# Kernel optimization log

Hardware: AMD Instinct MI355X
Metric: run time of the kernel (lower is better)

Reference implementation:

```python
import jax, jax.numpy as jnp
import numpy as np

N = 50000
E = 800000
H = 128


def _lin_init(key, fan_in, fan_out):
    s = 1.0 / np.sqrt(fan_in)
    k1, k2 = jax.random.split(key)
    W = jax.random.uniform(k1, (fan_in, fan_out), minval=-s, maxval=s, dtype=jnp.float32)
    b = jax.random.uniform(k2, (fan_out,), minval=-s, maxval=s, dtype=jnp.float32)
    return W, b


def setup_inputs() -> dict:
    key = jax.random.key(0)
    ks = jax.random.split(key, 24)
    inp = {}
    inp['x'] = jax.random.normal(ks[0], (N, 1), dtype=jnp.float32)
    inp['edge_attr'] = jax.random.normal(ks[1], (E, 1), dtype=jnp.float32)
    inp['q_Y_sample'] = jax.random.normal(ks[2], (E, 1), dtype=jnp.float32)
    inp['adj'] = jax.random.randint(ks[3], (2, E), 0, N, dtype=jnp.int32)
    inp['t'] = jax.random.uniform(ks[4], (1,), dtype=jnp.float32) * 1000.0
    inp['num_steps'] = 1000
    inp['batch'] = jnp.zeros((N,), dtype=jnp.int32)
    # parameters
    inp['We'], inp['be'] = _lin_init(ks[5], 1, H // 2)      # edge_map
    inp['Wo'], inp['bo'] = _lin_init(ks[6], 1, H // 2)      # edge_map_opt
    inp['Wl1'], inp['bl1'] = _lin_init(ks[7], H, 1)         # conv1 edge lin (edge_dim->in_channels)
    inp['Wn1'], inp['bn1'] = _lin_init(ks[8], 1, H)         # conv1 nn
    inp['Wl2'], inp['bl2'] = _lin_init(ks[9], H, H)         # conv2 edge lin
    inp['Wn2'], inp['bn2'] = _lin_init(ks[10], H, H)        # conv2 nn
    inp['Wl3'], inp['bl3'] = _lin_init(ks[11], H, H)        # conv3 edge lin
    inp['Wn3'], inp['bn3'] = _lin_init(ks[12], H, H)        # conv3 nn
    inp['Wt1'], inp['bt1'] = _lin_init(ks[13], H, 2 * H)    # time_mlp[0]
    inp['Wt2'], inp['bt2'] = _lin_init(ks[14], 2 * H, H)    # time_mlp[2]
    inp['Wd1'], inp['bd1'] = _lin_init(ks[15], 257, 257)    # decode[0]
    inp['Wd2'], inp['bd2'] = _lin_init(ks[16], 257, 1)      # decode[2]
    return inp


def reference(x, edge_attr, q_Y_sample, adj, t, num_steps, batch,
              We, be, Wo, bo,
              Wl1, bl1, Wn1, bn1, Wl2, bl2, Wn2, bn2, Wl3, bl3, Wn3, bn3,
              Wt1, bt1, Wt2, bt2, Wd1, bd1, Wd2, bd2):
    n = x.shape[0]
    src, dst = adj[0], adj[1]
    # edge embedding: cat(edge_map(edge_attr), edge_map_opt(q_Y_sample)) -> [E, 128]
    ee = jnp.concatenate([edge_attr @ We + be, q_Y_sample @ Wo + bo], axis=-1)
    # sinusoidal time embedding (t/num_steps*num_steps*rescale == 4*t)
    half = H // 2
    freqs = jnp.exp(jnp.arange(half, dtype=jnp.float32) * (-np.log(10000.0) / (half - 1)))
    tv = (t * 4.0)[:, None] * freqs[None, :]
    temb = jnp.concatenate([jnp.sin(tv), jnp.cos(tv)], axis=-1)  # [1, 128]
    temb = jax.nn.relu(temb @ Wt1 + bt1) @ Wt2 + bt2              # [1, 128], broadcasts to [N, 128]

    def gine(h, Wl, bl, Wn, bn):
        # PyG GINEConv (eps=0): out = nn(x + sum_j relu(x_j + lin(edge_attr)))
        m = jax.nn.relu(h[src] + (ee @ Wl + bl))                  # [E, d_in]
        agg = jax.ops.segment_sum(m, dst, num_segments=n)         # [N, d_in]
        return (h + agg) @ Wn + bn

    h = gine(x, Wl1, bl1, Wn1, bn1) + temb
    h = gine(h, Wl2, bl2, Wn2, bn2) + temb
    h = gine(h, Wl3, bl3, Wn3, bn3) + temb
    # decode on edges: cat(h[src], h[dst], q_Y_sample) -> MLP -> [E, 1]
    z = jnp.concatenate([h[src], h[dst], q_Y_sample], axis=-1)    # [E, 257]
    return jax.nn.relu(z @ Wd1 + bd1) @ Wd2 + bd2
```

## Files before the change

### kernel.cpp

```cpp
#include <hip/hip_runtime.h>

typedef unsigned int uint;
typedef unsigned short ushort;

#define AB_U 132

typedef __attribute__((ext_vector_type(8))) short short8;
typedef __attribute__((ext_vector_type(4))) float f32x4;
union U4S8 { uint4 u; short8 s; };

__device__ __forceinline__ ushort f2bf(float f) {
    uint u = __float_as_uint(f);
    u += 0x7FFFu + ((u >> 16) & 1u);
    return (ushort)(u >> 16);
}
__device__ __forceinline__ float bf2f_lo(uint p) { return __uint_as_float(p << 16); }
__device__ __forceinline__ float bf2f_hi(uint p) { return __uint_as_float(p & 0xFFFF0000u); }
__device__ __forceinline__ uint packbf(float lo, float hi) {
    return (uint)f2bf(lo) | ((uint)f2bf(hi) << 16);
}

__global__ __launch_bounds__(256) void precompute_kernel(
    const float* __restrict__ t,
    const float* __restrict__ We, const float* __restrict__ be,
    const float* __restrict__ Wo, const float* __restrict__ bo,
    const float* __restrict__ Wl1, const float* __restrict__ bl1,
    const float* __restrict__ Wl2, const float* __restrict__ bl2,
    const float* __restrict__ Wl3, const float* __restrict__ bl3,
    const float* __restrict__ Wt1, const float* __restrict__ bt1,
    const float* __restrict__ Wt2, const float* __restrict__ bt2,
    float* __restrict__ wsmall)
{
    __shared__ float t0[128];
    __shared__ float y1[256];
    int tid = threadIdx.x;
    float tt = t[0] * 4.0f;
    if (tid < 64) {
        float f = expf(-logf(10000.0f) * (float)tid / 63.0f);
        float v = tt * f;
        t0[tid]      = sinf(v);
        t0[tid + 64] = cosf(v);
    }
    __syncthreads();
    {
        float acc = bt1[tid];
        for (int k = 0; k < 128; k++) acc = fmaf(t0[k], Wt1[k * 256 + tid], acc);
        y1[tid] = fmaxf(acc, 0.0f);
    }
    __syncthreads();
    if (tid < 128) {
        float a = bt2[tid];
        for (int k = 0; k < 256; k++) a = fmaf(y1[k], Wt2[k * 128 + tid], a);
        wsmall[tid] = a;
    }
    {
        int j = tid & 127;
        const float* Wl  = (tid < 128) ? Wl2 : Wl3;
        const float* blp = (tid < 128) ? bl2 : bl3;
        float p = 0.f, q = 0.f, r = blp[j];
        for (int k = 0; k < 64; k++) {
            float w1 = Wl[k * 128 + j], w2 = Wl[(64 + k) * 128 + j];
            p = fmaf(We[k], w1, p);
            q = fmaf(Wo[k], w2, q);
            r = fmaf(be[k], w1, r);
            r = fmaf(bo[k], w2, r);
        }
        int base = (tid < 128) ? 128 : 512;
        wsmall[base + j]       = p;
        wsmall[base + 128 + j] = q;
        wsmall[base + 256 + j] = r;
    }
    if (tid == 0) {
        float p1 = 0.f, q1 = 0.f, r1 = bl1[0];
        for (int k = 0; k < 64; k++) {
            p1 = fmaf(We[k], Wl1[k], p1);
            q1 = fmaf(Wo[k], Wl1[64 + k], q1);
            r1 = fmaf(be[k], Wl1[k], r1);
            r1 = fmaf(bo[k], Wl1[64 + k], r1);
        }
        wsmall[896] = p1; wsmall[897] = q1; wsmall[898] = r1;
    }
}

__global__ __launch_bounds__(64) void wt16_kernel(
    const float* __restrict__ Wd1, uint* __restrict__ Wt16u)
{
    int c = blockIdx.x;
    int u = threadIdx.x;
    int k = u * 2;
    float lo, hi;
    if (c < 256) {
        lo = Wd1[k * 257 + c];
        hi = Wd1[(k + 1) * 257 + c];
    } else {
        int cc = c - 256;
        lo = Wd1[(128 + k) * 257 + cc];
        hi = Wd1[(128 + k + 1) * 257 + cc];
    }
    Wt16u[c * 64 + u] = packbf(lo, hi);
}

__global__ __launch_bounds__(256) void hist_kernel(
    const int* __restrict__ dst, int* __restrict__ cnt, int E)
{
    int e = blockIdx.x * blockDim.x + threadIdx.x;
    if (e < E) atomicAdd(&cnt[dst[e]], 1);
}

__global__ __launch_bounds__(256) void scan1_kernel(
    const int* __restrict__ cnt, int* __restrict__ rowstart,
    int* __restrict__ partials, int N)
{
    __shared__ int wsum[4];
    int b = blockIdx.x;
    int tid = threadIdx.x, lane = tid & 63, w = tid >> 6;
    int i0 = b * 1024 + tid * 4;
    int v0 = (i0     < N) ? cnt[i0]     : 0;
    int v1 = (i0 + 1 < N) ? cnt[i0 + 1] : 0;
    int v2 = (i0 + 2 < N) ? cnt[i0 + 2] : 0;
    int v3 = (i0 + 3 < N) ? cnt[i0 + 3] : 0;
    int tsum = v0 + v1 + v2 + v3;
    int s = tsum;
#pragma unroll
    for (int off = 1; off < 64; off <<= 1) {
        int u = __shfl_up(s, off, 64);
        if (lane >= off) s += u;
    }
    if (lane == 63) wsum[w] = s;
    __syncthreads();
    int woff = 0;
    for (int k = 0; k < w; k++) woff += wsum[k];
    int ex = woff + s - tsum;
    if (i0     < N) rowstart[i0]     = ex;
    if (i0 + 1 < N) rowstart[i0 + 1] = ex + v0;
    if (i0 + 2 < N) rowstart[i0 + 2] = ex + v0 + v1;
    if (i0 + 3 < N) rowstart[i0 + 3] = ex + v0 + v1 + v2;
    if (tid == 255) partials[b] = woff + s;
}

__global__ __launch_bounds__(64) void scan2_kernel(
    int* __restrict__ partials, int* __restrict__ rowstart, int nblk, int N)
{
    int lane = threadIdx.x;
    int carry = 0;
    for (int base = 0; base < nblk; base += 64) {
        int i = base + lane;
        int v = (i < nblk) ? partials[i] : 0;
        int s = v;
#pragma unroll
        for (int off = 1; off < 64; off <<= 1) {
            int u = __shfl_up(s, off, 64);
            if (lane >= off) s += u;
        }
        if (i < nblk) partials[i] = carry + s - v;
        carry += __shfl(s, 63, 64);
    }
    if (lane == 0) rowstart[N] = carry;
}

__global__ __launch_bounds__(256) void scan3_kernel(
    int* __restrict__ rowstart, const int* __restrict__ partials, int N)
{
    int i = blockIdx.x * blockDim.x + threadIdx.x;
    if (i < N) rowstart[i] += partials[i >> 10];
}

__global__ __launch_bounds__(256) void scatter_kernel(
    const int* __restrict__ src, const int* __restrict__ dst,
    const float* __restrict__ ea, const float* __restrict__ qy,
    const int* __restrict__ rowstart, int* __restrict__ cursor,
    uint4* __restrict__ epack, int E)
{
    int e = blockIdx.x * blockDim.x + threadIdx.x;
    if (e >= E) return;
    int d = dst[e];
    int pos = atomicAdd(&cursor[d], 1);
    uint4 pk;
    pk.x = (uint)e;
    pk.y = (uint)src[e];
    pk.z = __float_as_uint(ea[e]);
    pk.w = __float_as_uint(qy[e]);
    epack[rowstart[d] + pos] = pk;
}

__global__ __launch_bounds__(256) void edge1_kernel(
    const float* __restrict__ x, const uint4* __restrict__ epack,
    const int* __restrict__ rowstart, const float* __restrict__ scal,
    float* __restrict__ agg1, int N)
{
    int v = blockIdx.x * blockDim.x + threadIdx.x;
    if (v >= N) return;
    float s0 = scal[0], s1 = scal[1], s2 = scal[2];
    int beg = rowstart[v], end = rowstart[v + 1];
    float m = 0.0f;
    int i = beg;
    for (; i + 2 <= end; i += 2) {
        uint4 pk0 = epack[i];
        uint4 pk1 = epack[i + 1];
        float x0 = x[(int)pk0.y];
        float x1 = x[(int)pk1.y];
        m += fmaxf(x0 + fmaf(__uint_as_float(pk0.z), s0, fmaf(__uint_as_float(pk0.w), s1, s2)), 0.0f);
        m += fmaxf(x1 + fmaf(__uint_as_float(pk1.z), s0, fmaf(__uint_as_float(pk1.w), s1, s2)), 0.0f);
    }
    if (i < end) {
        uint4 pk = epack[i];
        m += fmaxf(x[(int)pk.y] + fmaf(__uint_as_float(pk.z), s0, fmaf(__uint_as_float(pk.w), s1, s2)), 0.0f);
    }
    agg1[v] = m;
}

__global__ __launch_bounds__(256) void node1_kernel(
    const float* __restrict__ x, const float* __restrict__ agg1,
    const float* __restrict__ Wn1, const float* __restrict__ bn1,
    const float* __restrict__ temb, float* __restrict__ h,
    uint* __restrict__ h16u, int N)
{
    int i = blockIdx.x * blockDim.x + threadIdx.x;
    int n = i >> 6, j2 = (i & 63) * 2;
    if (n >= N) return;
    float v = x[n] + agg1[n];
    float h0 = fmaf(v, Wn1[j2],     bn1[j2]     + temb[j2]);
    float h1 = fmaf(v, Wn1[j2 + 1], bn1[j2 + 1] + temb[j2 + 1]);
    *(float2*)(h + (size_t)n * 128 + j2) = make_float2(h0, h1);
    h16u[(size_t)n * 64 + (j2 >> 1)] = packbf(h0, h1);
}

__global__ __launch_bounds__(256) void aggL_kernel(
    const uint* __restrict__ h16u, const uint4* __restrict__ epack,
    const int* __restrict__ rowstart,
    const float* __restrict__ P, const float* __restrict__ Q,
    const float* __restrict__ R, float* __restrict__ agg, int N)
{
    int v = blockIdx.x * 4 + (threadIdx.x >> 6);
    int lane = threadIdx.x & 63;
    if (v >= N) return;
    int c = lane * 2;
    float2 Pv = *(const float2*)(P + c);
    float2 Qv = *(const float2*)(Q + c);
    float2 Rv = *(const float2*)(R + c);
    int beg = rowstart[v], end = rowstart[v + 1];
    float accx = 0.0f, accy = 0.0f;
    int i = beg;
    for (; i + 4 <= end; i += 4) {
        uint4 pk0 = epack[i];
        uint4 pk1 = epack[i + 1];
        uint4 pk2 = epack[i + 2];
        uint4 pk3 = epack[i + 3];
        uint hp0 = h16u[(size_t)pk0.y * 64 + lane];
        uint hp1 = h16u[(size_t)pk1.y * 64 + lane];
        uint hp2 = h16u[(size_t)pk2.y * 64 + lane];
        uint hp3 = h16u[(size_t)pk3.y * 64 + lane];
        float a0 = __uint_as_float(pk0.z), b0 = __uint_as_float(pk0.w);
        float a1 = __uint_as_float(pk1.z), b1 = __uint_as_float(pk1.w);
        float a2 = __uint_as_float(pk2.z), b2 = __uint_as_float(pk2.w);
        float a3 = __uint_as_float(pk3.z), b3 = __uint_as_float(pk3.w);
        accx += fmaxf(bf2f_lo(hp0) + fmaf(a0, Pv.x, fmaf(b0, Qv.x, Rv.x)), 0.0f);
        accy += fmaxf(bf2f_hi(hp0) + fmaf(a0, Pv.y, fmaf(b0, Qv.y, Rv.y)), 0.0f);
        accx += fmaxf(bf2f_lo(hp1) + fmaf(a1, Pv.x, fmaf(b1, Qv.x, Rv.x)), 0.0f);
        accy += fmaxf(bf2f_hi(hp1) + fmaf(a1, Pv.y, fmaf(b1, Qv.y, Rv.y)), 0.0f);
        accx += fmaxf(bf2f_lo(hp2) + fmaf(a2, Pv.x, fmaf(b2, Qv.x, Rv.x)), 0.0f);
        accy += fmaxf(bf2f_hi(hp2) + fmaf(a2, Pv.y, fmaf(b2, Qv.y, Rv.y)), 0.0f);
        accx += fmaxf(bf2f_lo(hp3) + fmaf(a3, Pv.x, fmaf(b3, Qv.x, Rv.x)), 0.0f);
        accy += fmaxf(bf2f_hi(hp3) + fmaf(a3, Pv.y, fmaf(b3, Qv.y, Rv.y)), 0.0f);
    }
    for (; i < end; i++) {
        uint4 pk = epack[i];
        float a = __uint_as_float(pk.z), b = __uint_as_float(pk.w);
        uint hp = h16u[(size_t)pk.y * 64 + lane];
        accx += fmaxf(bf2f_lo(hp) + fmaf(a, Pv.x, fmaf(b, Qv.x, Rv.x)), 0.0f);
        accy += fmaxf(bf2f_hi(hp) + fmaf(a, Pv.y, fmaf(b, Qv.y, Rv.y)), 0.0f);
    }
    *(float2*)(agg + (size_t)v * 128 + c) = make_float2(accx, accy);
}

__global__ __launch_bounds__(256) void nodeL_kernel(
    float* __restrict__ h, const float* __restrict__ agg,
    const float* __restrict__ W, const float* __restrict__ bn,
    const float* __restrict__ temb, uint* __restrict__ h16u, int N)
{
    __shared__ float vs[64][128];
    int nb = blockIdx.x * 64;
    int tid = threadIdx.x;
    for (int idx = tid; idx < 64 * 32; idx += 256) {
        int n = idx >> 5, c = (idx & 31) * 4;
        float4 a = make_float4(0.f, 0.f, 0.f, 0.f);
        if (nb + n < N) {
            a = *(const float4*)(h + (size_t)(nb + n) * 128 + c);
            float4 g = *(const float4*)(agg + (size_t)(nb + n) * 128 + c);
            a.x += g.x; a.y += g.y; a.z += g.z; a.w += g.w;
        }
        *(float4*)(&vs[n][c]) = a;
    }
    __syncthreads();
    int o0 = (tid & 31) * 4;
    int n0 = (tid >> 5) * 8;
    float acc[8][4];
    float4 bb = *(const float4*)(bn + o0);
    float4 tb = *(const float4*)(temb + o0);
    bb.x += tb.x; bb.y += tb.y; bb.z += tb.z; bb.w += tb.w;
#pragma unroll
    for (int i = 0; i < 8; i++) {
        acc[i][0] = bb.x; acc[i][1] = bb.y; acc[i][2] = bb.z; acc[i][3] = bb.w;
    }
    for (int k = 0; k < 128; k += 4) {
        float hv[8][4];
#pragma unroll
        for (int i = 0; i < 8; i++)
            *(float4*)hv[i] = *(const float4*)(&vs[n0 + i][k]);
#pragma unroll
        for (int kk = 0; kk < 4; kk++) {
            float4 wv = *(const float4*)(W + (k + kk) * 128 + o0);
#pragma unroll
            for (int i = 0; i < 8; i++) {
                float hvv = hv[i][kk];
                acc[i][0] = fmaf(hvv, wv.x, acc[i][0]);
                acc[i][1] = fmaf(hvv, wv.y, acc[i][1]);
                acc[i][2] = fmaf(hvv, wv.z, acc[i][2]);
                acc[i][3] = fmaf(hvv, wv.w, acc[i][3]);
            }
        }
    }
#pragma unroll
    for (int i = 0; i < 8; i++) {
        int n = nb + n0 + i;
        if (n < N) {
            *(float4*)(h + (size_t)n * 128 + o0) =
                make_float4(acc[i][0], acc[i][1], acc[i][2], acc[i][3]);
            uint2 pk;
            pk.x = packbf(acc[i][0], acc[i][1]);
            pk.y = packbf(acc[i][2], acc[i][3]);
            *(uint2*)(h16u + (size_t)n * 64 + (o0 >> 1)) = pk;
        }
    }
}

__global__ __launch_bounds__(256) void node3_decode_kernel(
    const float* __restrict__ h, const float* __restrict__ agg,
    const float* __restrict__ Wn3, const float* __restrict__ bn3,
    const float* __restrict__ temb, const uint* __restrict__ Wt16u,
    const float* __restrict__ Wd1, const float* __restrict__ bd1,
    ushort* __restrict__ A16s, ushort* __restrict__ B16s, int N)
{
    __shared__ float vs[16][128];
    __shared__ uint hs16[16][68];
    int nb = blockIdx.x * 16;
    int tid = threadIdx.x;
    for (int idx = tid; idx < 16 * 32; idx += 256) {
        int n = idx >> 5, c = (idx & 31) * 4;
        float4 a = make_float4(0.f, 0.f, 0.f, 0.f);
        if (nb + n < N) {
            a = *(const float4*)(h + (size_t)(nb + n) * 128 + c);
            float4 g = *(const float4*)(agg + (size_t)(nb + n) * 128 + c);
            a.x += g.x; a.y += g.y; a.z += g.z; a.w += g.w;
        }
        *(float4*)(&vs[n][c]) = a;
    }
    __syncthreads();
    {
        int o0 = (tid & 31) * 4;
        int n0 = (tid >> 5) * 2;
        float acc[2][4];
        float4 bb = *(const float4*)(bn3 + o0);
        float4 tb = *(const float4*)(temb + o0);
        bb.x += tb.x; bb.y += tb.y; bb.z += tb.z; bb.w += tb.w;
#pragma unroll
        for (int i = 0; i < 2; i++) {
            acc[i][0] = bb.x; acc[i][1] = bb.y; acc[i][2] = bb.z; acc[i][3] = bb.w;
        }
        for (int k = 0; k < 128; k += 4) {
            float hv0[4], hv1[4];
            *(float4*)hv0 = *(const float4*)(&vs[n0][k]);
            *(float4*)hv1 = *(const float4*)(&vs[n0 + 1][k]);
#pragma unroll
            for (int kk = 0; kk < 4; kk++) {
                float4 wv = *(const float4*)(Wn3 + (k + kk) * 128 + o0);
                acc[0][0] = fmaf(hv0[kk], wv.x, acc[0][0]);
                acc[0][1] = fmaf(hv0[kk], wv.y, acc[0][1]);
                acc[0][2] = fmaf(hv0[kk], wv.z, acc[0][2]);
                acc[0][3] = fmaf(hv0[kk], wv.w, acc[0][3]);
                acc[1][0] = fmaf(hv1[kk], wv.x, acc[1][0]);
                acc[1][1] = fmaf(hv1[kk], wv.y, acc[1][1]);
                acc[1][2] = fmaf(hv1[kk], wv.z, acc[1][2]);
                acc[1][3] = fmaf(hv1[kk], wv.w, acc[1][3]);
            }
        }
#pragma unroll
        for (int i = 0; i < 2; i++) {
            uint2 pk;
            pk.x = packbf(acc[i][0], acc[i][1]);
            pk.y = packbf(acc[i][2], acc[i][3]);
            *(uint2*)(&hs16[n0 + i][o0 >> 1]) = pk;
        }
    }
    __syncthreads();
    {
        int wv = tid >> 6;
        int lane = tid & 63;
        int cl = lane & 15;
        int g = lane >> 4;
        short8 afr[4];
#pragma unroll
        for (int kc = 0; kc < 4; kc++) {
            U4S8 t;
            t.u = *(const uint4*)(&hs16[cl][kc * 16 + g * 4]);
            afr[kc] = t.s;
        }
#pragma unroll
        for (int tt = 0; tt < 8; tt++) {
            int tile = wv * 8 + tt;
            int c = tile * 16 + cl;
            float bias = (tile < 16) ? bd1[c] : 0.0f;
            f32x4 acc = {bias, bias, bias, bias};
#pragma unroll
            for (int kc = 0; kc < 4; kc++) {
                U4S8 t;
                t.u = *(const uint4*)(Wt16u + (size_t)c * 64 + kc * 16 + g * 4);
                acc = __builtin_amdgcn_mfma_f32_16x16x32_bf16(afr[kc], t.s, acc, 0, 0, 0);
            }
            ushort* OUT = (tile < 16) ? A16s : B16s;
            int oc = (tile < 16) ? c : (c - 256);
#pragma unroll
            for (int r = 0; r < 4; r++) {
                int n = nb + g * 4 + r;
                if (n < N) OUT[(size_t)n * 264 + oc] = f2bf(acc[r]);
            }
        }
    }
    if (tid < 16) {
        int n = tid;
        float sA = bd1[256], sB = 0.f;
        for (int u = 0; u < 64; u++) {
            uint pk = hs16[n][u];
            float h0 = bf2f_lo(pk), h1 = bf2f_hi(pk);
            int k = u * 2;
            sA = fmaf(h0, Wd1[k * 257 + 256], sA);
            sA = fmaf(h1, Wd1[(k + 1) * 257 + 256], sA);
            sB = fmaf(h0, Wd1[(128 + k) * 257 + 256], sB);
            sB = fmaf(h1, Wd1[(128 + k + 1) * 257 + 256], sB);
        }
        if (nb + n < N) {
            A16s[(size_t)(nb + n) * 264 + 256] = f2bf(sA);
            B16s[(size_t)(nb + n) * 264 + 256] = f2bf(sB);
        }
    }
}

__global__ __launch_bounds__(256) void decodeE_kernel(
    const uint* __restrict__ A16u, const uint* __restrict__ B16u,
    const uint4* __restrict__ epack, const int* __restrict__ rowstart,
    const float* __restrict__ Wd1, const float* __restrict__ Wd2,
    const float* __restrict__ bd2, float* __restrict__ out, int N)
{
    int v = blockIdx.x * 4 + (threadIdx.x >> 6);
    int lane = threadIdx.x & 63;
    if (v >= N) return;
    const float* w256 = Wd1 + 256 * 257;
    float4 w2v = *(const float4*)(w256 + lane * 4);
    float4 wdv = *(const float4*)(Wd2 + lane * 4);
    const uint* Br = B16u + (size_t)v * AB_U;
    uint2 bp = *(const uint2*)(Br + lane * 2);
    float Bv0 = bf2f_lo(bp.x), Bv1 = bf2f_hi(bp.x);
    float Bv2 = bf2f_lo(bp.y), Bv3 = bf2f_hi(bp.y);
    float w2_l = w256[256], wd_l = Wd2[256], bd = bd2[0];
    float B_l = bf2f_lo(Br[128]);
    int beg = rowstart[v], end = rowstart[v + 1];
    int i = beg;
    for (; i + 2 <= end; i += 2) {
        uint4 pk0 = epack[i];
        uint4 pk1 = epack[i + 1];
        float q0 = __uint_as_float(pk0.w);
        float q1 = __uint_as_float(pk1.w);
        const uint* Ar0 = A16u + (size_t)pk0.y * AB_U;
        const uint* Ar1 = A16u + (size_t)pk1.y * AB_U;
        uint2 ap0 = *(const uint2*)(Ar0 + lane * 2);
        uint2 ap1 = *(const uint2*)(Ar1 + lane * 2);
        float t0 = 0.f, t1 = 0.f;
        if (lane == 0) {
            t0 = bf2f_lo(Ar0[128]);
            t1 = bf2f_lo(Ar1[128]);
        }
        float y00 = bf2f_lo(ap0.x) + fmaf(q0, w2v.x, Bv0);
        float y01 = bf2f_hi(ap0.x) + fmaf(q0, w2v.y, Bv1);
        float y02 = bf2f_lo(ap0.y) + fmaf(q0, w2v.z, Bv2);
        float y03 = bf2f_hi(ap0.y) + fmaf(q0, w2v.w, Bv3);
        float acc0 = fmaxf(y00, 0.f) * wdv.x + fmaxf(y01, 0.f) * wdv.y
                   + fmaxf(y02, 0.f) * wdv.z + fmaxf(y03, 0.f) * wdv.w;
        float y10 = bf2f_lo(ap1.x) + fmaf(q1, w2v.x, Bv0);
        float y11 = bf2f_hi(ap1.x) + fmaf(q1, w2v.y, Bv1);
        float y12 = bf2f_lo(ap1.y) + fmaf(q1, w2v.z, Bv2);
        float y13 = bf2f_hi(ap1.y) + fmaf(q1, w2v.w, Bv3);
        float acc1 = fmaxf(y10, 0.f) * wdv.x + fmaxf(y11, 0.f) * wdv.y
                   + fmaxf(y12, 0.f) * wdv.z + fmaxf(y13, 0.f) * wdv.w;
        if (lane == 0) {
            acc0 = fmaf(fmaxf(t0 + fmaf(q0, w2_l, B_l), 0.f), wd_l, acc0);
            acc1 = fmaf(fmaxf(t1 + fmaf(q1, w2_l, B_l), 0.f), wd_l, acc1);
        }
#pragma unroll
        for (int off = 32; off > 0; off >>= 1) {
            acc0 += __shfl_xor(acc0, off, 64);
            acc1 += __shfl_xor(acc1, off, 64);
        }
        if (lane == 0) {
            out[(int)pk0.x] = acc0 + bd;
            out[(int)pk1.x] = acc1 + bd;
        }
    }
    if (i < end) {
        uint4 pk = epack[i];
        float q = __uint_as_float(pk.w);
        const uint* Ar = A16u + (size_t)pk.y * AB_U;
        uint2 ap = *(const uint2*)(Ar + lane * 2);
        float y0 = bf2f_lo(ap.x) + fmaf(q, w2v.x, Bv0);
        float y1 = bf2f_hi(ap.x) + fmaf(q, w2v.y, Bv1);
        float y2 = bf2f_lo(ap.y) + fmaf(q, w2v.z, Bv2);
        float y3 = bf2f_hi(ap.y) + fmaf(q, w2v.w, Bv3);
        float acc = fmaxf(y0, 0.f) * wdv.x + fmaxf(y1, 0.f) * wdv.y
                  + fmaxf(y2, 0.f) * wdv.z + fmaxf(y3, 0.f) * wdv.w;
        if (lane == 0) {
            float yl = bf2f_lo(Ar[128]) + fmaf(q, w2_l, B_l);
            acc = fmaf(fmaxf(yl, 0.f), wd_l, acc);
        }
#pragma unroll
        for (int off = 32; off > 0; off >>= 1) acc += __shfl_xor(acc, off, 64);
        if (lane == 0) out[(int)pk.x] = acc + bd;
    }
}

extern "C" void kernel_launch(void* const* d_in, const int* in_sizes, int n_in,
                              void* d_out, int out_size, void* d_ws, size_t ws_size,
                              hipStream_t stream) {
    (void)n_in; (void)out_size; (void)ws_size;
    const float* x   = (const float*)d_in[0];
    const float* ea  = (const float*)d_in[1];
    const float* qy  = (const float*)d_in[2];
    const int*   adj = (const int*)d_in[3];
    const float* t   = (const float*)d_in[4];
    const float* We  = (const float*)d_in[7];
    const float* be  = (const float*)d_in[8];
    const float* Wo  = (const float*)d_in[9];
    const float* bo  = (const float*)d_in[10];
    const float* Wl1 = (const float*)d_in[11];
    const float* bl1 = (const float*)d_in[12];
    const float* Wn1 = (const float*)d_in[13];
    const float* bn1 = (const float*)d_in[14];
    const float* Wl2 = (const float*)d_in[15];
    const float* bl2 = (const float*)d_in[16];
    const float* Wn2 = (const float*)d_in[17];
    const float* bn2 = (const float*)d_in[18];
    const float* Wl3 = (const float*)d_in[19];
    const float* bl3 = (const float*)d_in[20];
    const float* Wn3 = (const float*)d_in[21];
    const float* bn3 = (const float*)d_in[22];
    const float* Wt1 = (const float*)d_in[23];
    const float* bt1 = (const float*)d_in[24];
    const float* Wt2 = (const float*)d_in[25];
    const float* bt2 = (const float*)d_in[26];
    const float* Wd1 = (const float*)d_in[27];
    const float* bd1 = (const float*)d_in[28];
    const float* Wd2 = (const float*)d_in[29];
    const float* bd2 = (const float*)d_in[30];
    float* out = (float*)d_out;

    int N = in_sizes[0];
    int E = in_sizes[3] / 2;
    const int* src = adj;
    const int* dst = adj + E;

    float* w    = (float*)d_ws;
    float* temb = w;
    float* P2   = w + 128;
    float* Q2   = w + 256;
    float* R2   = w + 384;
    float* P3   = w + 512;
    float* Q3   = w + 640;
    float* R3   = w + 768;
    float* scal = w + 896;
    float* h    = w + 1024;
    float* agg  = h + (size_t)N * 128;
    uint*  h16u = (uint*)(agg + (size_t)N * 128);
    uint*  A16u = h16u + (size_t)N * 64;
    uint*  B16u = A16u + (size_t)N * AB_U;
    int* rowstart = (int*)(B16u + (size_t)N * AB_U);
    int* cursor   = rowstart + (N + 1);
    int* partials = cursor + N;
    int nblk = (N + 1023) / 1024;
    char* pcur = (char*)(partials + nblk + 1);
    pcur = (char*)(((uintptr_t)pcur + 15) & ~(uintptr_t)15);
    uint4* epack = (uint4*)pcur;
    uint* Wt16u = (uint*)(epack + E);

    hipMemsetAsync(cursor, 0, (size_t)N * sizeof(int), stream);
    hist_kernel<<<(E + 255) / 256, 256, 0, stream>>>(dst, cursor, E);
    scan1_kernel<<<nblk, 256, 0, stream>>>(cursor, rowstart, partials, N);
    scan2_kernel<<<1, 64, 0, stream>>>(partials, rowstart, nblk, N);
    scan3_kernel<<<(N + 255) / 256, 256, 0, stream>>>(rowstart, partials, N);
    hipMemsetAsync(cursor, 0, (size_t)N * sizeof(int), stream);
    scatter_kernel<<<(E + 255) / 256, 256, 0, stream>>>(src, dst, ea, qy, rowstart, cursor, epack, E);

    wt16_kernel<<<512, 64, 0, stream>>>(Wd1, Wt16u);
    precompute_kernel<<<1, 256, 0, stream>>>(t, We, be, Wo, bo, Wl1, bl1,
                                             Wl2, bl2, Wl3, bl3,
                                             Wt1, bt1, Wt2, bt2, w);
    edge1_kernel<<<(N + 255) / 256, 256, 0, stream>>>(x, epack, rowstart, scal, agg, N);
    node1_kernel<<<(N * 64 + 255) / 256, 256, 0, stream>>>(x, agg, Wn1, bn1, temb, h, h16u, N);
    aggL_kernel<<<(N + 3) / 4, 256, 0, stream>>>(h16u, epack, rowstart, P2, Q2, R2, agg, N);
    nodeL_kernel<<<(N + 63) / 64, 256, 0, stream>>>(h, agg, Wn2, bn2, temb, h16u, N);
    aggL_kernel<<<(N + 3) / 4, 256, 0, stream>>>(h16u, epack, rowstart, P3, Q3, R3, agg, N);
    node3_decode_kernel<<<(N + 15) / 16, 256, 0, stream>>>(h, agg, Wn3, bn3, temb, Wt16u,
                                                           Wd1, bd1,
                                                           (ushort*)A16u, (ushort*)B16u, N);
    decodeE_kernel<<<(N + 3) / 4, 256, 0, stream>>>(A16u, B16u, epack, rowstart, Wd1, Wd2, bd2, out, N);
}
```

Baseline: 573.5 us.

## Use bf16 MFMA for node GEMMs and keep hidden/aggregate state in bf16

Replaces the fp32 FMA loops in the layer-2 and layer-3 node linear layers with bf16 MFMA 16x16x32 instructions, using pre-transposed bf16 copies of Wn2 and Wn3 made by a new small kernel. The fp32 node-state buffer is removed and the aggregation output is stored as packed bf16, roughly halving that write and read traffic. The node-3 decode path now keeps the layer-3 result in fp32 shared memory and splits the extra-column dot product across 64 threads with shuffles. This trades accuracy, since hidden state and aggregates are rounded to bf16 at more points, for less memory traffic and compute in the node stages.

```diff
diff --git a/kernel.cpp b/kernel.cpp
--- a/kernel.cpp
+++ b/kernel.cpp
@@ -98,6 +98,13 @@
         hi = Wd1[(128 + k + 1) * 257 + cc];
     }
     Wt16u[c * 64 + u] = packbf(lo, hi);
+}
+
+__global__ __launch_bounds__(64) void wnt16_kernel(
+    const float* __restrict__ W, uint* __restrict__ Wt)
+{
+    int c = blockIdx.x, u = threadIdx.x;
+    Wt[c * 64 + u] = packbf(W[(2 * u) * 128 + c], W[(2 * u + 1) * 128 + c]);
 }
 
 __global__ __launch_bounds__(256) void hist_kernel(
@@ -212,8 +219,7 @@
 __global__ __launch_bounds__(256) void node1_kernel(
     const float* __restrict__ x, const float* __restrict__ agg1,
     const float* __restrict__ Wn1, const float* __restrict__ bn1,
-    const float* __restrict__ temb, float* __restrict__ h,
-    uint* __restrict__ h16u, int N)
+    const float* __restrict__ temb, uint* __restrict__ h16u, int N)
 {
     int i = blockIdx.x * blockDim.x + threadIdx.x;
     int n = i >> 6, j2 = (i & 63) * 2;
@@ -221,7 +227,6 @@
     float v = x[n] + agg1[n];
     float h0 = fmaf(v, Wn1[j2],     bn1[j2]     + temb[j2]);
     float h1 = fmaf(v, Wn1[j2 + 1], bn1[j2 + 1] + temb[j2 + 1]);
-    *(float2*)(h + (size_t)n * 128 + j2) = make_float2(h0, h1);
     h16u[(size_t)n * 64 + (j2 >> 1)] = packbf(h0, h1);
 }
 
@@ -229,7 +234,7 @@
     const uint* __restrict__ h16u, const uint4* __restrict__ epack,
     const int* __restrict__ rowstart,
     const float* __restrict__ P, const float* __restrict__ Q,
-    const float* __restrict__ R, float* __restrict__ agg, int N)
+    const float* __restrict__ R, uint* __restrict__ agg16u, int N)
 {
     int v = blockIdx.x * 4 + (threadIdx.x >> 6);
     int lane = threadIdx.x & 63;
@@ -270,139 +275,119 @@
         accx += fmaxf(bf2f_lo(hp) + fmaf(a, Pv.x, fmaf(b, Qv.x, Rv.x)), 0.0f);
         accy += fmaxf(bf2f_hi(hp) + fmaf(a, Pv.y, fmaf(b, Qv.y, Rv.y)), 0.0f);
     }
-    *(float2*)(agg + (size_t)v * 128 + c) = make_float2(accx, accy);
+    agg16u[(size_t)v * 64 + lane] = packbf(accx, accy);
 }
 
 __global__ __launch_bounds__(256) void nodeL_kernel(
-    float* __restrict__ h, const float* __restrict__ agg,
-    const float* __restrict__ W, const float* __restrict__ bn,
-    const float* __restrict__ temb, uint* __restrict__ h16u, int N)
-{
-    __shared__ float vs[64][128];
+    const uint* __restrict__ agg16u, const uint* __restrict__ Wn2t16u,
+    const float* __restrict__ bn, const float* __restrict__ temb,
+    uint* __restrict__ h16u, int N)
+{
+    __shared__ uint vs16[64][68];
     int nb = blockIdx.x * 64;
     int tid = threadIdx.x;
     for (int idx = tid; idx < 64 * 32; idx += 256) {
-        int n = idx >> 5, c = (idx & 31) * 4;
-        float4 a = make_float4(0.f, 0.f, 0.f, 0.f);
+        int n = idx >> 5, u2 = (idx & 31) * 2;
+        uint2 pk = make_uint2(0, 0);
         if (nb + n < N) {
-            a = *(const float4*)(h + (size_t)(nb + n) * 128 + c);
-            float4 g = *(const float4*)(agg + (size_t)(nb + n) * 128 + c);
-            a.x += g.x; a.y += g.y; a.z += g.z; a.w += g.w;
-        }
-        *(float4*)(&vs[n][c]) = a;
+            uint2 hp = *(const uint2*)(h16u + (size_t)(nb + n) * 64 + u2);
+            uint2 gp = *(const uint2*)(agg16u + (size_t)(nb + n) * 64 + u2);
+            pk.x = packbf(bf2f_lo(hp.x) + bf2f_lo(gp.x), bf2f_hi(hp.x) + bf2f_hi(gp.x));
+            pk.y = packbf(bf2f_lo(hp.y) + bf2f_lo(gp.y), bf2f_hi(hp.y) + bf2f_hi(gp.y));
+        }
+        *(uint2*)(&vs16[n][u2]) = pk;
     }
     __syncthreads();
-    int o0 = (tid & 31) * 4;
-    int n0 = (tid >> 5) * 8;
-    float acc[8][4];
-    float4 bb = *(const float4*)(bn + o0);
-    float4 tb = *(const float4*)(temb + o0);
-    bb.x += tb.x; bb.y += tb.y; bb.z += tb.z; bb.w += tb.w;
-#pragma unroll
-    for (int i = 0; i < 8; i++) {
-        acc[i][0] = bb.x; acc[i][1] = bb.y; acc[i][2] = bb.z; acc[i][3] = bb.w;
-    }
-    for (int k = 0; k < 128; k += 4) {
-        float hv[8][4];
-#pragma unroll
-        for (int i = 0; i < 8; i++)
-            *(float4*)hv[i] = *(const float4*)(&vs[n0 + i][k]);
-#pragma unroll
-        for (int kk = 0; kk < 4; kk++) {
-            float4 wv = *(const float4*)(W + (k + kk) * 128 + o0);
-#pragma unroll
-            for (int i = 0; i < 8; i++) {
-                float hvv = hv[i][kk];
-                acc[i][0] = fmaf(hvv, wv.x, acc[i][0]);
-                acc[i][1] = fmaf(hvv, wv.y, acc[i][1]);
-                acc[i][2] = fmaf(hvv, wv.z, acc[i][2]);
-                acc[i][3] = fmaf(hvv, wv.w, acc[i][3]);
-            }
-        }
-    }
-#pragma unroll
-    for (int i = 0; i < 8; i++) {
-        int n = nb + n0 + i;
-        if (n < N) {
-            *(float4*)(h + (size_t)n * 128 + o0) =
-                make_float4(acc[i][0], acc[i][1], acc[i][2], acc[i][3]);
-            uint2 pk;
-            pk.x = packbf(acc[i][0], acc[i][1]);
-            pk.y = packbf(acc[i][2], acc[i][3]);
-            *(uint2*)(h16u + (size_t)n * 64 + (o0 >> 1)) = pk;
+    int wv = tid >> 6, lane = tid & 63, cl = lane & 15, g = lane >> 4;
+    int rbase = wv * 16;
+    short8 afr[4];
+#pragma unroll
+    for (int kc = 0; kc < 4; kc++) {
+        U4S8 t;
+        t.u = *(const uint4*)(&vs16[rbase + cl][kc * 16 + g * 4]);
+        afr[kc] = t.s;
+    }
+#pragma unroll
+    for (int tt = 0; tt < 8; tt++) {
+        int c = tt * 16 + cl;
+        float bias = bn[c] + temb[c];
+        f32x4 acc = {bias, bias, bias, bias};
+#pragma unroll
+        for (int kc = 0; kc < 4; kc++) {
+            U4S8 t;
+            t.u = *(const uint4*)(Wn2t16u + (size_t)c * 64 + kc * 16 + g * 4);
+            acc = __builtin_amdgcn_mfma_f32_16x16x32_bf16(afr[kc], t.s, acc, 0, 0, 0);
+        }
+#pragma unroll
+        for (int r = 0; r < 4; r++) {
+            int n = nb + rbase + g * 4 + r;
+            float val = acc[r];
+            float nbr = __shfl_down(val, 1, 64);
+            if (n < N && (cl & 1) == 0)
+                h16u[(size_t)n * 64 + (c >> 1)] = packbf(val, nbr);
         }
     }
 }
 
 __global__ __launch_bounds__(256) void node3_decode_kernel(
-    const float* __restrict__ h, const float* __restrict__ agg,
-    const float* __restrict__ Wn3, const float* __restrict__ bn3,
+    const uint* __restrict__ h16u, const uint* __restrict__ agg16u,
+    const uint* __restrict__ Wn3t16u, const float* __restrict__ bn3,
     const float* __restrict__ temb, const uint* __restrict__ Wt16u,
     const float* __restrict__ Wd1, const float* __restrict__ bd1,
     ushort* __restrict__ A16s, ushort* __restrict__ B16s, int N)
 {
-    __shared__ float vs[16][128];
-    __shared__ uint hs16[16][68];
+    __shared__ uint vs16[16][68];
+    __shared__ float hs3[16][132];
     int nb = blockIdx.x * 16;
     int tid = threadIdx.x;
     for (int idx = tid; idx < 16 * 32; idx += 256) {
-        int n = idx >> 5, c = (idx & 31) * 4;
-        float4 a = make_float4(0.f, 0.f, 0.f, 0.f);
+        int n = idx >> 5, u2 = (idx & 31) * 2;
+        uint2 pk = make_uint2(0, 0);
         if (nb + n < N) {
-            a = *(const float4*)(h + (size_t)(nb + n) * 128 + c);
-            float4 g = *(const float4*)(agg + (size_t)(nb + n) * 128 + c);
-            a.x += g.x; a.y += g.y; a.z += g.z; a.w += g.w;
-        }
-        *(float4*)(&vs[n][c]) = a;
+            uint2 hp = *(const uint2*)(h16u + (size_t)(nb + n) * 64 + u2);
+            uint2 gp = *(const uint2*)(agg16u + (size_t)(nb + n) * 64 + u2);
+            pk.x = packbf(bf2f_lo(hp.x) + bf2f_lo(gp.x), bf2f_hi(hp.x) + bf2f_hi(gp.x));
+            pk.y = packbf(bf2f_lo(hp.y) + bf2f_lo(gp.y), bf2f_hi(hp.y) + bf2f_hi(gp.y));
+        }
+        *(uint2*)(&vs16[n][u2]) = pk;
+    }
+    __syncthreads();
+    int wv = tid >> 6, lane = tid & 63, cl = lane & 15, g = lane >> 4;
+    {
+        short8 afr[4];
+#pragma unroll
+        for (int kc = 0; kc < 4; kc++) {
+            U4S8 t;
+            t.u = *(const uint4*)(&vs16[cl][kc * 16 + g * 4]);
+            afr[kc] = t.s;
+        }
+#pragma unroll
+        for (int tt = 0; tt < 2; tt++) {
+            int c = wv * 32 + tt * 16 + cl;
+            float bias = bn3[c] + temb[c];
+            f32x4 acc = {bias, bias, bias, bias};
+#pragma unroll
+            for (int kc = 0; kc < 4; kc++) {
+                U4S8 t;
+                t.u = *(const uint4*)(Wn3t16u + (size_t)c * 64 + kc * 16 + g * 4);
+                acc = __builtin_amdgcn_mfma_f32_16x16x32_bf16(afr[kc], t.s, acc, 0, 0, 0);
+            }
+#pragma unroll
+            for (int r = 0; r < 4; r++) hs3[g * 4 + r][c] = acc[r];
+        }
     }
     __syncthreads();
     {
-        int o0 = (tid & 31) * 4;
-        int n0 = (tid >> 5) * 2;
-        float acc[2][4];
-        float4 bb = *(const float4*)(bn3 + o0);
-        float4 tb = *(const float4*)(temb + o0);
-        bb.x += tb.x; bb.y += tb.y; bb.z += tb.z; bb.w += tb.w;
-#pragma unroll
-        for (int i = 0; i < 2; i++) {
-            acc[i][0] = bb.x; acc[i][1] = bb.y; acc[i][2] = bb.z; acc[i][3] = bb.w;
-        }
-        for (int k = 0; k < 128; k += 4) {
-            float hv0[4], hv1[4];
-            *(float4*)hv0 = *(const float4*)(&vs[n0][k]);
-            *(float4*)hv1 = *(const float4*)(&vs[n0 + 1][k]);
-#pragma unroll
-            for (int kk = 0; kk < 4; kk++) {
-                float4 wv = *(const float4*)(Wn3 + (k + kk) * 128 + o0);
-                acc[0][0] = fmaf(hv0[kk], wv.x, acc[0][0]);
-                acc[0][1] = fmaf(hv0[kk], wv.y, acc[0][1]);
-                acc[0][2] = fmaf(hv0[kk], wv.z, acc[0][2]);
-                acc[0][3] = fmaf(hv0[kk], wv.w, acc[0][3]);
-                acc[1][0] = fmaf(hv1[kk], wv.x, acc[1][0]);
-                acc[1][1] = fmaf(hv1[kk], wv.y, acc[1][1]);
-                acc[1][2] = fmaf(hv1[kk], wv.z, acc[1][2]);
-                acc[1][3] = fmaf(hv1[kk], wv.w, acc[1][3]);
-            }
-        }
-#pragma unroll
-        for (int i = 0; i < 2; i++) {
-            uint2 pk;
-            pk.x = packbf(acc[i][0], acc[i][1]);
-            pk.y = packbf(acc[i][2], acc[i][3]);
-            *(uint2*)(&hs16[n0 + i][o0 >> 1]) = pk;
-        }
-    }
-    __syncthreads();
-    {
-        int wv = tid >> 6;
-        int lane = tid & 63;
-        int cl = lane & 15;
-        int g = lane >> 4;
         short8 afr[4];
 #pragma unroll
         for (int kc = 0; kc < 4; kc++) {
+            float4 lo = *(const float4*)(&hs3[cl][kc * 32 + g * 8]);
+            float4 hi = *(const float4*)(&hs3[cl][kc * 32 + g * 8 + 4]);
             U4S8 t;
-            t.u = *(const uint4*)(&hs16[cl][kc * 16 + g * 4]);
+            t.u.x = packbf(lo.x, lo.y);
+            t.u.y = packbf(lo.z, lo.w);
+            t.u.z = packbf(hi.x, hi.y);
+            t.u.w = packbf(hi.z, hi.w);
             afr[kc] = t.s;
         }
 #pragma unroll
@@ -426,20 +411,20 @@
             }
         }
     }
-    if (tid < 16) {
-        int n = tid;
-        float sA = bd1[256], sB = 0.f;
-        for (int u = 0; u < 64; u++) {
-            uint pk = hs16[n][u];
-            float h0 = bf2f_lo(pk), h1 = bf2f_hi(pk);
-            int k = u * 2;
-            sA = fmaf(h0, Wd1[k * 257 + 256], sA);
-            sA = fmaf(h1, Wd1[(k + 1) * 257 + 256], sA);
-            sB = fmaf(h0, Wd1[(128 + k) * 257 + 256], sB);
-            sB = fmaf(h1, Wd1[(128 + k + 1) * 257 + 256], sB);
-        }
-        if (nb + n < N) {
-            A16s[(size_t)(nb + n) * 264 + 256] = f2bf(sA);
+    if (tid < 64) {
+        int n = tid >> 2, j = tid & 3;
+        float sA = 0.f, sB = 0.f;
+        for (int k = j * 32; k < j * 32 + 32; k++) {
+            float hv = hs3[n][k];
+            sA = fmaf(hv, Wd1[k * 257 + 256], sA);
+            sB = fmaf(hv, Wd1[(128 + k) * 257 + 256], sB);
+        }
+        sA += __shfl_xor(sA, 1, 64);
+        sA += __shfl_xor(sA, 2, 64);
+        sB += __shfl_xor(sB, 1, 64);
+        sB += __shfl_xor(sB, 2, 64);
+        if (j == 0 && nb + n < N) {
+            A16s[(size_t)(nb + n) * 264 + 256] = f2bf(sA + bd1[256]);
             B16s[(size_t)(nb + n) * 264 + 256] = f2bf(sB);
         }
     }
@@ -575,11 +560,11 @@
     float* Q3   = w + 640;
     float* R3   = w + 768;
     float* scal = w + 896;
-    float* h    = w + 1024;
-    float* agg  = h + (size_t)N * 128;
-    uint*  h16u = (uint*)(agg + (size_t)N * 128);
-    uint*  A16u = h16u + (size_t)N * 64;
-    uint*  B16u = A16u + (size_t)N * AB_U;
+    float* agg1 = w + 1024;
+    uint*  h16u   = (uint*)(agg1 + N);
+    uint*  agg16u = h16u + (size_t)N * 64;
+    uint*  A16u   = agg16u + (size_t)N * 64;
+    uint*  B16u   = A16u + (size_t)N * AB_U;
     int* rowstart = (int*)(B16u + (size_t)N * AB_U);
     int* cursor   = rowstart + (N + 1);
     int* partials = cursor + N;
@@ -587,7 +572,9 @@
     char* pcur = (char*)(partials + nblk + 1);
     pcur = (char*)(((uintptr_t)pcur + 15) & ~(uintptr_t)15);
     uint4* epack = (uint4*)pcur;
-    uint* Wt16u = (uint*)(epack + E);
+    uint* Wt16u   = (uint*)(epack + E);
+    uint* Wn2t16u = Wt16u + 512 * 64;
+    uint* Wn3t16u = Wn2t16u + 128 * 64;
 
     hipMemsetAsync(cursor, 0, (size_t)N * sizeof(int), stream);
     hist_kernel<<<(E + 255) / 256, 256, 0, stream>>>(dst, cursor, E);
@@ -598,16 +585,18 @@
     scatter_kernel<<<(E + 255) / 256, 256, 0, stream>>>(src, dst, ea, qy, rowstart, cursor, epack, E);
 
     wt16_kernel<<<512, 64, 0, stream>>>(Wd1, Wt16u);
+    wnt16_kernel<<<128, 64, 0, stream>>>(Wn2, Wn2t16u);
+    wnt16_kernel<<<128, 64, 0, stream>>>(Wn3, Wn3t16u);
     precompute_kernel<<<1, 256, 0, stream>>>(t, We, be, Wo, bo, Wl1, bl1,
                                              Wl2, bl2, Wl3, bl3,
                                              Wt1, bt1, Wt2, bt2, w);
-    edge1_kernel<<<(N + 255) / 256, 256, 0, stream>>>(x, epack, rowstart, scal, agg, N);
-    node1_kernel<<<(N * 64 + 255) / 256, 256, 0, stream>>>(x, agg, Wn1, bn1, temb, h, h16u, N);
-    aggL_kernel<<<(N + 3) / 4, 256, 0, stream>>>(h16u, epack, rowstart, P2, Q2, R2, agg, N);
-    nodeL_kernel<<<(N + 63) / 64, 256, 0, stream>>>(h, agg, Wn2, bn2, temb, h16u, N);
-    aggL_kernel<<<(N + 3) / 4, 256, 0, stream>>>(h16u, epack, rowstart, P3, Q3, R3, agg, N);
-    node3_decode_kernel<<<(N + 15) / 16, 256, 0, stream>>>(h, agg, Wn3, bn3, temb, Wt16u,
-                                                           Wd1, bd1,
+    edge1_kernel<<<(N + 255) / 256, 256, 0, stream>>>(x, epack, rowstart, scal, agg1, N);
+    node1_kernel<<<(N * 64 + 255) / 256, 256, 0, stream>>>(x, agg1, Wn1, bn1, temb, h16u, N);
+    aggL_kernel<<<(N + 3) / 4, 256, 0, stream>>>(h16u, epack, rowstart, P2, Q2, R2, agg16u, N);
+    nodeL_kernel<<<(N + 63) / 64, 256, 0, stream>>>(agg16u, Wn2t16u, bn2, temb, h16u, N);
+    aggL_kernel<<<(N + 3) / 4, 256, 0, stream>>>(h16u, epack, rowstart, P3, Q3, R3, agg16u, N);
+    node3_decode_kernel<<<(N + 15) / 16, 256, 0, stream>>>(h16u, agg16u, Wn3t16u, bn3, temb,
+                                                           Wt16u, Wd1, bd1,
                                                            (ushort*)A16u, (ushort*)B16u, N);
     decodeE_kernel<<<(N + 3) / 4, 256, 0, stream>>>(A16u, B16u, epack, rowstart, Wd1, Wd2, bd2, out, N);
 }
```

Measured after the change: 530.7 us. 1.08x faster.
